# Kernel optimization log

Measured on AMD Instinct MI355X. Metric: run time of the kernel, lower is better.

The kernel has to match this reference:

```python
import jax, jax.numpy as jnp
import numpy as np
import math

THETA = 10000.0

def apply_rope(x):
    # x: [B, H, S, D] with D even; interleaved even/odd rotation
    B, H, S, D = x.shape
    dim_half = D // 2
    freq_idx = jnp.arange(dim_half, dtype=jnp.float32)
    inv_freq = jnp.exp(-math.log(THETA) * freq_idx * 2.0 / D)  # [D/2]
    pos = jnp.arange(S, dtype=jnp.float32)
    angles = pos[:, None] * inv_freq[None, :]      # [S, D/2]
    cos = jnp.cos(angles)[None, None]              # [1,1,S,D/2]
    sin = jnp.sin(angles)[None, None]
    x_even = x[..., ::2]
    x_odd = x[..., 1::2]
    r_even = x_even * cos - x_odd * sin
    r_odd = x_odd * cos + x_even * sin
    return jnp.stack([r_even, r_odd], axis=-1).reshape(B, H, S, D)

def setup_inputs() -> dict:
    key = jax.random.key(0)
    ks = jax.random.split(key, 5)
    B, S, E = 2, 2048, 1024
    std = 0.02
    inp = {
        "hidden_states": jax.random.normal(ks[0], (B, S, E), dtype=jnp.float32),
        "Wq": jax.random.normal(ks[1], (E, E), dtype=jnp.float32) * std,
        "bq": jnp.zeros((E,), dtype=jnp.float32),
        "Wk": jax.random.normal(ks[2], (E, E), dtype=jnp.float32) * std,
        "bk": jnp.zeros((E,), dtype=jnp.float32),
        "Wv": jax.random.normal(ks[3], (E, E), dtype=jnp.float32) * std,
        "bv": jnp.zeros((E,), dtype=jnp.float32),
        "Wo": jax.random.normal(ks[4], (E, E), dtype=jnp.float32) * std,
        "bo": jnp.zeros((E,), dtype=jnp.float32),
    }
    return inp

def reference(hidden_states, Wq, bq, Wk, bk, Wv, bv, Wo, bo):
    NUM_HEADS = 16
    B, S, E = hidden_states.shape
    D = E // NUM_HEADS
    scale = 1.0 / math.sqrt(D)

    def proj(W, b):
        # torch Linear: x @ W.T + b; then [B,S,H,D] -> [B,H,S,D]
        y = hidden_states @ W.T + b
        return y.reshape(B, S, NUM_HEADS, D).transpose(0, 2, 1, 3)

    q = apply_rope(proj(Wq, bq))
    k = apply_rope(proj(Wk, bk))
    v = proj(Wv, bv)

    scores = jnp.einsum("bhqd,bhkd->bhqk", q, k) * scale
    attn = jax.nn.softmax(scores, axis=-1)
    out = jnp.einsum("bhqk,bhkd->bhqd", attn, v)  # [B,H,S,D]
    out = out.transpose(0, 2, 1, 3).reshape(B, S, E)
    return out @ Wo.T + bo  # dropout: eval mode (identity)
```

## Files before the change

kernel.cpp:

```cpp
#include <hip/hip_runtime.h>
#include <hip/hip_bf16.h>
#include <math.h>

#define B_ 2
#define S_ 2048
#define E_ 1024
#define H_ 16
#define D_ 64
#define M_ (B_*S_)
#define PT 32

typedef short bf16x8 __attribute__((ext_vector_type(8)));
typedef float f32x4 __attribute__((ext_vector_type(4)));
typedef unsigned short u16x4 __attribute__((ext_vector_type(4)));

#define SCLQ 0.18033688011112042f

__device__ __forceinline__ unsigned short f2bf(float f) {
    unsigned int u = __builtin_bit_cast(unsigned int, f);
    u += 0x7FFFu + ((u >> 16) & 1u);
    return (unsigned short)(u >> 16);
}
__device__ __forceinline__ unsigned int pk2bf(float a, float b) {
    __hip_bfloat162 h = __float22bfloat162_rn(make_float2(a, b));
    unsigned int u;
    __builtin_memcpy(&u, &h, 4);
    return u;
}
__device__ __forceinline__ f32x4 mfma16(bf16x8 a, bf16x8 b, f32x4 c) {
    return __builtin_amdgcn_mfma_f32_16x16x32_bf16(a, b, c, 0, 0, 0);
}
__device__ __forceinline__ bf16x8 cvt8(const float* p) {
    f32x4 lo = *(const f32x4*)p;
    f32x4 hi = *(const f32x4*)(p + 4);
    unsigned int pk[4];
    pk[0] = pk2bf(lo[0], lo[1]);
    pk[1] = pk2bf(lo[2], lo[3]);
    pk[2] = pk2bf(hi[0], hi[1]);
    pk[3] = pk2bf(hi[2], hi[3]);
    bf16x8 r;
    __builtin_memcpy(&r, pk, 16);
    return r;
}
__device__ __forceinline__ void g2l16(const unsigned short* g, unsigned short* l) {
    __builtin_amdgcn_global_load_lds(
        (const __attribute__((address_space(1))) unsigned int*)(const void*)g,
        (__attribute__((address_space(3))) unsigned int*)(void*)l,
        16, 0, 0);
}

__global__ __launch_bounds__(256) void cvt_kernel(
    const float* __restrict__ X,  const float* __restrict__ Wq,
    const float* __restrict__ Wk, const float* __restrict__ Wv,
    const float* __restrict__ Wo,
    unsigned short* __restrict__ Xb, unsigned short* __restrict__ Wb,
    float* __restrict__ tab)
{
    const int y = blockIdx.y;
    if (y == 5) {
        unsigned int i = blockIdx.x * 256 + threadIdx.x;
        if (i < 32 * 2048) {
            int f = i >> 11, s = i & 2047;
            const float C = -0.41524101186091903f;
            const float INV2PI = 0.15915494309189535f;
            float inv_rev = exp2f(C * (float)f) * INV2PI;
            float rev = (float)s * inv_rev;
            float fr = rev - rintf(rev);
            tab[i]           = __builtin_amdgcn_cosf(fr);
            tab[65536 + i]   = __builtin_amdgcn_sinf(fr);
        }
        return;
    }
    const float* src = (y == 0) ? X : (y == 1) ? Wq : (y == 2) ? Wk : (y == 3) ? Wv : Wo;
    unsigned short* dst = (y == 0) ? Xb : Wb + (size_t)(y - 1) * (E_ * E_);
    const size_t n = (y == 0) ? (size_t)M_ * E_ : (size_t)E_ * E_;
    size_t i = ((size_t)blockIdx.x * 256 + threadIdx.x) * 8;
    if (i < n) *(bf16x8*)(dst + i) = cvt8(src + i);
}

__global__ __launch_bounds__(256, 4) void qkv_rope_bf(
    const unsigned short* __restrict__ Xb, const unsigned short* __restrict__ Wb,
    const float* __restrict__ bq, const float* __restrict__ bk,
    const float* __restrict__ bv, const float* __restrict__ tab,
    unsigned short* __restrict__ Qo, unsigned short* __restrict__ Ko,
    unsigned short* __restrict__ Vo)
{
    __shared__ __align__(16) unsigned char lds_raw[128 * 132 * 2];
    unsigned short* As = (unsigned short*)lds_raw;
    unsigned short* Bs = (unsigned short*)(lds_raw + 16384);
    unsigned short* Cs = (unsigned short*)lds_raw;

    const int t = threadIdx.x;
    const int w = t >> 6, lane = t & 63, quad = lane >> 4, l16 = lane & 15;
    const int wr = (w >> 1) * 64, wc = (w & 1) * 64;

    const int wgid = blockIdx.x + ((blockIdx.y + (blockIdx.z << 5)) << 3);
    const int sw = (wgid & 7) * 96 + (wgid >> 3);
    const int n0 = (sw & 7) * 128;
    const int rem = sw >> 3;
    const int m0 = (rem & 31) * 128;
    const int z = rem >> 5;

    const unsigned short* W = Wb + (size_t)z * (E_ * E_);
    const float* bias = (z == 0) ? bq : (z == 1) ? bk : bv;

    const int r8 = t >> 3;
    const int scol = ((t & 7) ^ ((t >> 3) & 7)) * 8;
    const unsigned short* Ag = Xb + (size_t)(m0 + r8) * E_ + scol;
    const unsigned short* Bg = W  + (size_t)(n0 + r8) * E_ + scol;

    const int sw0 = ((quad)     ^ (l16 & 7)) * 8;
    const int sw1 = ((4 + quad) ^ (l16 & 7)) * 8;

    f32x4 zero = {0.f, 0.f, 0.f, 0.f};
    f32x4 acc[4][4];
#pragma unroll
    for (int i = 0; i < 4; i++)
#pragma unroll
        for (int j = 0; j < 4; j++) acc[i][j] = zero;

    for (int kt = 0; kt < E_; kt += 64) {
        __syncthreads();
#pragma unroll
        for (int c = 0; c < 4; c++) {
            g2l16(Ag + kt + (size_t)(c * 32) * E_, &As[t * 8 + c * 2048]);
            g2l16(Bg + kt + (size_t)(c * 32) * E_, &Bs[t * 8 + c * 2048]);
        }
        __syncthreads();
#pragma unroll
        for (int ks = 0; ks < 2; ks++) {
            const int so = ks ? sw1 : sw0;
            bf16x8 af[4], bfr[4];
#pragma unroll
            for (int i = 0; i < 4; i++)
                af[i] = *(const bf16x8*)&As[(wr + i * 16 + l16) * 64 + so];
#pragma unroll
            for (int j = 0; j < 4; j++)
                bfr[j] = *(const bf16x8*)&Bs[(wc + j * 16 + l16) * 64 + so];
#pragma unroll
            for (int i = 0; i < 4; i++)
#pragma unroll
                for (int j = 0; j < 4; j++)
                    acc[i][j] = mfma16(af[i], bfr[j], acc[i][j]);
        }
    }

    __syncthreads();
    const int seg = quad;
    if (z < 2) {
        const float qscale = (z == 0) ? SCLQ : 1.0f;
#pragma unroll
        for (int j = 0; j < 4; j++) {
            int n_local = wc + j * 16 + l16;
            int n = n0 + n_local;
            int d = n & 63, f = d >> 1;
            float bvv = bias[n];
            float sgn = (d & 1) ? 1.f : -1.f;
            const float* ct = tab + f * 2048;
            const float* st_ = tab + 65536 + f * 2048;
#pragma unroll
            for (int i = 0; i < 4; i++) {
                int mb = wr + i * 16 + quad * 4;
                int sb = (m0 + mb) & (S_ - 1);
                f32x4 cs4 = *(const f32x4*)&ct[sb];
                f32x4 sn4 = *(const f32x4*)&st_[sb];
#pragma unroll
                for (int r = 0; r < 4; r++) {
                    float val = acc[i][j][r] + bvv;
                    float oth = __shfl_xor(val, 1);
                    Cs[(mb + r) * 132 + n_local] =
                        f2bf((val * cs4[r] + sgn * oth * sn4[r]) * qscale);
                }
            }
        }
        __syncthreads();
        unsigned short* Out = (z == 0) ? Qo : Ko;
        const int btok = m0 >> 11;
        const int half = seg & 1;
#pragma unroll
        for (int it = 0; it < 16; it++) {
            int m_local = it * 8 + w * 2 + (seg >> 1);
            int s = (m0 + m_local) & (S_ - 1);
            int h = (n0 + half * 64) >> 6;
            u16x4 v = *(const u16x4*)&Cs[m_local * 132 + half * 64 + l16 * 4];
            *(u16x4*)&Out[(((size_t)btok * H_ + h) * S_ + s) * D_ + l16 * 4] = v;
        }
    } else {
#pragma unroll
        for (int j = 0; j < 4; j++) {
            int n_local = wc + j * 16 + l16;
            float bvv = bias[n0 + n_local];
#pragma unroll
            for (int i = 0; i < 4; i++) {
                int mb = wr + i * 16 + quad * 4;
#pragma unroll
                for (int r = 0; r < 4; r++)
                    Cs[n_local * 132 + mb + r] = f2bf(acc[i][j][r] + bvv);
            }
        }
        __syncthreads();
        const int btok = m0 >> 11;
        const int s0 = m0 & (S_ - 1);
        const int half = seg & 1;
#pragma unroll
        for (int it = 0; it < 16; it++) {
            int n_local = it * 8 + w * 2 + (seg >> 1);
            int n = n0 + n_local;
            int h = n >> 6, d = n & 63;
            u16x4 v = *(const u16x4*)&Cs[n_local * 132 + half * 64 + l16 * 4];
            *(u16x4*)&Vo[(((size_t)btok * H_ + h) * D_ + d) * S_ + s0 + half * 64 + l16 * 4] = v;
        }
    }
}

__global__ __launch_bounds__(512, 2) void attn_direct(
    const unsigned short* __restrict__ Q, const unsigned short* __restrict__ K,
    const unsigned short* __restrict__ Vt, unsigned short* __restrict__ ctx)
{
    __shared__ unsigned short Ks[3][64 * 64];
    __shared__ unsigned short Vs[3][64 * 64];
    __shared__ unsigned short Ps[8][16 * 72];
    const int t = threadIdx.x;
    const int w = t >> 6, lane = t & 63, quad = lane >> 4, l16 = lane & 15;

    const int wgid = blockIdx.x + (blockIdx.y << 4);
    const int sw = (wgid & 7) * 64 + (wgid >> 3);
    const int bh = sw >> 4;
    const int q0 = (sw & 15) * 128 + w * 16;
    const int NT = S_ / 64;

    const unsigned short* Qg = Q + ((size_t)bh * S_ + q0) * D_;
    bf16x8 qf[2];
#pragma unroll
    for (int ks = 0; ks < 2; ks++)
        qf[ks] = *(const bf16x8*)(Qg + (size_t)l16 * 64 + ks * 32 + quad * 8);

    bf16x8 ones;
#pragma unroll
    for (int e = 0; e < 8; e++) ones[e] = (short)0x3F80;

    f32x4 zero = {0.f, 0.f, 0.f, 0.f};
    f32x4 acc_o[4];
    f32x4 acc_l = zero;
#pragma unroll
    for (int j = 0; j < 4; j++) acc_o[j] = zero;

    const int tt = t & 255, ksel = t >> 8;
    const int sr = tt >> 2;
    const int sc = ((tt & 3) ^ ((tt >> 3) & 3)) * 8;
    const unsigned short* KgL = K  + (size_t)bh * S_ * D_ + (size_t)sr * 64 + ksel * 32 + sc;
    const unsigned short* VgL = Vt + (size_t)bh * D_ * S_ + (size_t)sr * S_ + ksel * 32 + sc;

    const int sl = (quad ^ ((l16 >> 1) & 3)) * 8;

    g2l16(KgL, &Ks[0][t * 8]);
    g2l16(VgL, &Vs[0][t * 8]);
    __syncthreads();
    g2l16(KgL + 4096, &Ks[1][t * 8]);
    g2l16(VgL + 64,   &Vs[1][t * 8]);
    {
        f32x4 sc4[4];
#pragma unroll
        for (int j = 0; j < 4; j++) sc4[j] = zero;
#pragma unroll
        for (int ks = 0; ks < 2; ks++)
#pragma unroll
            for (int j = 0; j < 4; j++) {
                bf16x8 kf = *(const bf16x8*)&Ks[0][ks * 2048 + (j * 16 + l16) * 32 + sl];
                sc4[j] = mfma16(qf[ks], kf, sc4[j]);
            }
#pragma unroll
        for (int j = 0; j < 4; j++)
#pragma unroll
            for (int r = 0; r < 4; r += 2) {
                float pa = __builtin_amdgcn_exp2f(sc4[j][r]);
                float pb = __builtin_amdgcn_exp2f(sc4[j][r + 1]);
                unsigned int u = pk2bf(pa, pb);
                Ps[w][(quad * 4 + r)     * 72 + j * 16 + l16] = (unsigned short)u;
                Ps[w][(quad * 4 + r + 1) * 72 + j * 16 + l16] = (unsigned short)(u >> 16);
            }
    }

    int bc = 0, bn = 1, bx = 2;
    for (int i = 0; i < NT - 1; ++i) {
        __syncthreads();
        if (i + 2 < NT) {
            g2l16(KgL + (size_t)(i + 2) * 4096, &Ks[bx][t * 8]);
            g2l16(VgL + (i + 2) * 64,           &Vs[bx][t * 8]);
        }
        bf16x8 pf0 = *(const bf16x8*)&Ps[w][l16 * 72 + quad * 8];
        bf16x8 pf1 = *(const bf16x8*)&Ps[w][l16 * 72 + 32 + quad * 8];

        __builtin_amdgcn_s_setprio(1);
        f32x4 scn[4];
#pragma unroll
        for (int j = 0; j < 4; j++) scn[j] = zero;
#pragma unroll
        for (int ks = 0; ks < 2; ks++)
#pragma unroll
            for (int j = 0; j < 4; j++) {
                bf16x8 kf = *(const bf16x8*)&Ks[bn][ks * 2048 + (j * 16 + l16) * 32 + sl];
                scn[j] = mfma16(qf[ks], kf, scn[j]);
            }
#pragma unroll
        for (int jd = 0; jd < 4; jd++) {
            bf16x8 vf = *(const bf16x8*)&Vs[bc][(jd * 16 + l16) * 32 + sl];
            acc_o[jd] = mfma16(pf0, vf, acc_o[jd]);
        }
        acc_l = mfma16(pf0, ones, acc_l);
#pragma unroll
        for (int jd = 0; jd < 4; jd++) {
            bf16x8 vf = *(const bf16x8*)&Vs[bc][2048 + (jd * 16 + l16) * 32 + sl];
            acc_o[jd] = mfma16(pf1, vf, acc_o[jd]);
        }
        acc_l = mfma16(pf1, ones, acc_l);
        __builtin_amdgcn_s_setprio(0);

#pragma unroll
        for (int j = 0; j < 4; j++)
#pragma unroll
            for (int r = 0; r < 4; r += 2) {
                float pa = __builtin_amdgcn_exp2f(scn[j][r]);
                float pb = __builtin_amdgcn_exp2f(scn[j][r + 1]);
                unsigned int u = pk2bf(pa, pb);
                Ps[w][(quad * 4 + r)     * 72 + j * 16 + l16] = (unsigned short)u;
                Ps[w][(quad * 4 + r + 1) * 72 + j * 16 + l16] = (unsigned short)(u >> 16);
            }

        int tb = bc; bc = bn; bn = bx; bx = tb;
    }

    {
        bf16x8 pf0 = *(const bf16x8*)&Ps[w][l16 * 72 + quad * 8];
        bf16x8 pf1 = *(const bf16x8*)&Ps[w][l16 * 72 + 32 + quad * 8];
#pragma unroll
        for (int jd = 0; jd < 4; jd++) {
            bf16x8 vf = *(const bf16x8*)&Vs[bc][(jd * 16 + l16) * 32 + sl];
            acc_o[jd] = mfma16(pf0, vf, acc_o[jd]);
        }
        acc_l = mfma16(pf0, ones, acc_l);
#pragma unroll
        for (int jd = 0; jd < 4; jd++) {
            bf16x8 vf = *(const bf16x8*)&Vs[bc][2048 + (jd * 16 + l16) * 32 + sl];
            acc_o[jd] = mfma16(pf1, vf, acc_o[jd]);
        }
        acc_l = mfma16(pf1, ones, acc_l);
    }

    const int b = bh >> 4, h = bh & 15;
    f32x4 rl;
#pragma unroll
    for (int r = 0; r < 4; r++) rl[r] = 1.0f / acc_l[r];
#pragma unroll
    for (int jd = 0; jd < 4; jd++)
#pragma unroll
        for (int r = 0; r < 4; r++) {
            int qrow = q0 + quad * 4 + r;
            int col = h * 64 + jd * 16 + l16;
            ctx[((size_t)b * S_ + qrow) * E_ + col] = f2bf(acc_o[jd][r] * rl[r]);
        }
}

__global__ __launch_bounds__(256, 4) void out_bf(
    const unsigned short* __restrict__ Cx, const unsigned short* __restrict__ Wob,
    const float* __restrict__ bo, float* __restrict__ out)
{
    __shared__ unsigned short As[128 * 64];
    __shared__ unsigned short Bs[64 * 64];
    const int t = threadIdx.x;
    const int w = t >> 6, lane = t & 63, quad = lane >> 4, l16 = lane & 15;

    const int wgid = blockIdx.x + (blockIdx.y << 4);
    const int sw = (wgid & 7) * 64 + (wgid >> 3);
    const int n0 = (sw & 15) * 64;
    const int m0 = (sw >> 4) * 128;

    const int wr = w * 32;
    const int r8 = t >> 3;
    const int scol = ((t & 7) ^ ((t >> 3) & 7)) * 8;
    const unsigned short* Ag = Cx  + (size_t)(m0 + r8) * E_ + scol;
    const unsigned short* Bg = Wob + (size_t)(n0 + (r8 & 63)) * E_ + scol;

    const int sw0 = ((quad)     ^ (l16 & 7)) * 8;
    const int sw1 = ((4 + quad) ^ (l16 & 7)) * 8;

    f32x4 zero = {0.f, 0.f, 0.f, 0.f};
    f32x4 acc[2][4];
#pragma unroll
    for (int i = 0; i < 2; i++)
#pragma unroll
        for (int j = 0; j < 4; j++) acc[i][j] = zero;

    for (int kt = 0; kt < E_; kt += 64) {
        __syncthreads();
#pragma unroll
        for (int c = 0; c < 4; c++)
            g2l16(Ag + kt + (size_t)(c * 32) * E_, &As[t * 8 + c * 2048]);
#pragma unroll
        for (int c = 0; c < 2; c++)
            g2l16(Bg + kt + (size_t)(c * 32) * E_, &Bs[t * 8 + c * 2048]);
        __syncthreads();
#pragma unroll
        for (int ks = 0; ks < 2; ks++) {
            const int so = ks ? sw1 : sw0;
            bf16x8 af[2], bfr[4];
#pragma unroll
            for (int i = 0; i < 2; i++)
                af[i] = *(const bf16x8*)&As[(wr + i * 16 + l16) * 64 + so];
#pragma unroll
            for (int j = 0; j < 4; j++)
                bfr[j] = *(const bf16x8*)&Bs[(j * 16 + l16) * 64 + so];
#pragma unroll
            for (int i = 0; i < 2; i++)
#pragma unroll
                for (int j = 0; j < 4; j++)
                    acc[i][j] = mfma16(af[i], bfr[j], acc[i][j]);
        }
    }

#pragma unroll
    for (int j = 0; j < 4; j++) {
        int n = n0 + j * 16 + l16;
        float bvv = bo[n];
#pragma unroll
        for (int i = 0; i < 2; i++) {
            int mrow = m0 + wr + i * 16 + quad * 4;
#pragma unroll
            for (int r = 0; r < 4; r++)
                out[(size_t)(mrow + r) * E_ + n] = acc[i][j][r] + bvv;
        }
    }
}

__global__ __launch_bounds__(256, 3) void qkv_rope_f32(
    const float* __restrict__ X,
    const float* __restrict__ Wq, const float* __restrict__ Wk,
    const float* __restrict__ Wv,
    const float* __restrict__ bq, const float* __restrict__ bk,
    const float* __restrict__ bv,
    unsigned short* __restrict__ Qo, unsigned short* __restrict__ Ko,
    unsigned short* __restrict__ Vo)
{
    __shared__ __align__(16) unsigned char lds_raw[128 * 132 * 2];
    unsigned short* As = (unsigned short*)lds_raw;
    unsigned short* Bs = (unsigned short*)(lds_raw + 8192);
    unsigned short* Cs = (unsigned short*)lds_raw;

    const int t = threadIdx.x;
    const int w = t >> 6, lane = t & 63, quad = lane >> 4, l16 = lane & 15;
    const int wr = (w >> 1) * 64, wc = (w & 1) * 64;
    const int n0 = blockIdx.x * 128, m0 = blockIdx.y * 128;
    const int z = blockIdx.z;
    const float* W    = (z == 0) ? Wq : (z == 1) ? Wk : Wv;
    const float* bias = (z == 0) ? bq : (z == 1) ? bk : bv;

    const int r4 = t >> 2, c8 = (t & 3) * 8;
    const int st = r4 * PT + c8;
    const float* Ag = X + (size_t)(m0 + r4) * E_ + c8;
    const float* Bg = W + (size_t)(n0 + r4) * E_ + c8;

    f32x4 zero = {0.f, 0.f, 0.f, 0.f};
    f32x4 acc[4][4];
#pragma unroll
    for (int i = 0; i < 4; i++)
#pragma unroll
        for (int j = 0; j < 4; j++) acc[i][j] = zero;

    for (int kt = 0; kt < E_; kt += 32) {
        bf16x8 a0 = cvt8(Ag + kt);
        bf16x8 a1 = cvt8(Ag + 64 * E_ + kt);
        bf16x8 b0 = cvt8(Bg + kt);
        bf16x8 b1 = cvt8(Bg + 64 * E_ + kt);
        __syncthreads();
        *(bf16x8*)&As[st]           = a0;
        *(bf16x8*)&As[st + 64 * PT] = a1;
        *(bf16x8*)&Bs[st]           = b0;
        *(bf16x8*)&Bs[st + 64 * PT] = b1;
        __syncthreads();
        bf16x8 af[4], bfr[4];
#pragma unroll
        for (int i = 0; i < 4; i++)
            af[i] = *(const bf16x8*)&As[(wr + i * 16 + l16) * PT + quad * 8];
#pragma unroll
        for (int j = 0; j < 4; j++)
            bfr[j] = *(const bf16x8*)&Bs[(wc + j * 16 + l16) * PT + quad * 8];
#pragma unroll
        for (int i = 0; i < 4; i++)
#pragma unroll
            for (int j = 0; j < 4; j++)
                acc[i][j] = mfma16(af[i], bfr[j], acc[i][j]);
    }

    __syncthreads();
    const int seg = quad;
    if (z < 2) {
        const float C = -0.41524101186091903f;
        const float INV2PI = 0.15915494309189535f;
        const float qscale = (z == 0) ? SCLQ : 1.0f;
#pragma unroll
        for (int j = 0; j < 4; j++) {
            int n_local = wc + j * 16 + l16;
            int n = n0 + n_local;
            int d = n & 63, f = d >> 1;
            float inv_rev = exp2f(C * (float)f) * INV2PI;
            float bvv = bias[n];
            float sgn = (d & 1) ? 1.f : -1.f;
#pragma unroll
            for (int i = 0; i < 4; i++) {
                int mb = wr + i * 16 + quad * 4;
#pragma unroll
                for (int r = 0; r < 4; r++) {
                    int m = m0 + mb + r;
                    int s = m & (S_ - 1);
                    float val = acc[i][j][r] + bvv;
                    float oth = __shfl_xor(val, 1);
                    float rev = (float)s * inv_rev;
                    float fr = rev - rintf(rev);
                    float sn = __builtin_amdgcn_sinf(fr);
                    float cs = __builtin_amdgcn_cosf(fr);
                    Cs[(mb + r) * 132 + n_local] =
                        f2bf((val * cs + sgn * oth * sn) * qscale);
                }
            }
        }
        __syncthreads();
        unsigned short* Out = (z == 0) ? Qo : Ko;
        const int btok = m0 >> 11;
        const int half = seg & 1;
#pragma unroll
        for (int it = 0; it < 16; it++) {
            int m_local = it * 8 + w * 2 + (seg >> 1);
            int s = (m0 + m_local) & (S_ - 1);
            int h = (n0 + half * 64) >> 6;
            u16x4 v = *(const u16x4*)&Cs[m_local * 132 + half * 64 + l16 * 4];
            *(u16x4*)&Out[(((size_t)btok * H_ + h) * S_ + s) * D_ + l16 * 4] = v;
        }
    } else {
#pragma unroll
        for (int j = 0; j < 4; j++) {
            int n_local = wc + j * 16 + l16;
            float bvv = bias[n0 + n_local];
#pragma unroll
            for (int i = 0; i < 4; i++) {
                int mb = wr + i * 16 + quad * 4;
#pragma unroll
                for (int r = 0; r < 4; r++)
                    Cs[n_local * 132 + mb + r] = f2bf(acc[i][j][r] + bvv);
            }
        }
        __syncthreads();
        const int btok = m0 >> 11;
        const int s0 = m0 & (S_ - 1);
        const int half = seg & 1;
#pragma unroll
        for (int it = 0; it < 16; it++) {
            int n_local = it * 8 + w * 2 + (seg >> 1);
            int n = n0 + n_local;
            int h = n >> 6, d = n & 63;
            u16x4 v = *(const u16x4*)&Cs[n_local * 132 + half * 64 + l16 * 4];
            *(u16x4*)&Vo[(((size_t)btok * H_ + h) * D_ + d) * S_ + s0 + half * 64 + l16 * 4] = v;
        }
    }
}

__global__ __launch_bounds__(256, 2) void out_f32(
    const unsigned short* __restrict__ Cx, const float* __restrict__ Wo,
    const float* __restrict__ bo, float* __restrict__ out)
{
    __shared__ unsigned short As[128 * PT];
    __shared__ unsigned short Bs[64 * PT];
    const int t = threadIdx.x;
    const int w = t >> 6, lane = t & 63, quad = lane >> 4, l16 = lane & 15;
    const int m0 = blockIdx.y * 128, n0 = blockIdx.x * 64;
    const int wr = w * 32;
    const int r4 = t >> 2, c8 = (t & 3) * 8;
    const int st = r4 * PT + c8;
    const unsigned short* Ag = Cx + (size_t)(m0 + r4) * E_ + c8;
    const float*          Bg = Wo + (size_t)(n0 + (r4 & 63)) * E_ + c8;

    f32x4 zero = {0.f, 0.f, 0.f, 0.f};
    f32x4 acc[2][4];
#pragma unroll
    for (int i = 0; i < 2; i++)
#pragma unroll
        for (int j = 0; j < 4; j++) acc[i][j] = zero;

    for (int kt = 0; kt < E_; kt += 32) {
        bf16x8 a0 = *(const bf16x8*)(Ag + kt);
        bf16x8 a1 = *(const bf16x8*)(Ag + 64 * E_ + kt);
        bf16x8 b0 = cvt8(Bg + kt);
        __syncthreads();
        *(bf16x8*)&As[st]           = a0;
        *(bf16x8*)&As[st + 64 * PT] = a1;
        *(bf16x8*)&Bs[st]           = b0;
        __syncthreads();
        bf16x8 af[2], bfr[4];
#pragma unroll
        for (int i = 0; i < 2; i++)
            af[i] = *(const bf16x8*)&As[(wr + i * 16 + l16) * PT + quad * 8];
#pragma unroll
        for (int j = 0; j < 4; j++)
            bfr[j] = *(const bf16x8*)&Bs[(j * 16 + l16) * PT + quad * 8];
#pragma unroll
        for (int i = 0; i < 2; i++)
#pragma unroll
            for (int j = 0; j < 4; j++)
                acc[i][j] = mfma16(af[i], bfr[j], acc[i][j]);
    }

#pragma unroll
    for (int j = 0; j < 4; j++) {
        int n = n0 + j * 16 + l16;
        float bvv = bo[n];
#pragma unroll
        for (int i = 0; i < 2; i++) {
            int mrow = m0 + wr + i * 16 + quad * 4;
#pragma unroll
            for (int r = 0; r < 4; r++)
                out[(size_t)(mrow + r) * E_ + n] = acc[i][j][r] + bvv;
        }
    }
}

extern "C" void kernel_launch(void* const* d_in, const int* in_sizes, int n_in,
                              void* d_out, int out_size, void* d_ws, size_t ws_size,
                              hipStream_t stream) {
    const float* X  = (const float*)d_in[0];
    const float* Wq = (const float*)d_in[1];
    const float* bq = (const float*)d_in[2];
    const float* Wk = (const float*)d_in[3];
    const float* bk = (const float*)d_in[4];
    const float* Wv = (const float*)d_in[5];
    const float* bv = (const float*)d_in[6];
    const float* Wo = (const float*)d_in[7];
    const float* bo = (const float*)d_in[8];
    float* outp = (float*)d_out;

    const size_t TN = (size_t)B_ * H_ * S_ * D_;
    const size_t need_f32 = 4 * TN * sizeof(unsigned short);
    const size_t need_bf  = 5 * TN * sizeof(unsigned short) + 2 * 65536 * sizeof(float);
    if (ws_size < need_f32) return;

    unsigned short* Qb = (unsigned short*)d_ws;
    unsigned short* Kb = Qb + TN;
    unsigned short* Vb = Kb + TN;

    if (ws_size >= need_bf) {
        unsigned short* Xb = Vb + TN;
        unsigned short* Wb = Xb + TN;
        float* tab = (float*)(Wb + 4 * (size_t)(E_ * E_));
        unsigned short* Cx = Xb;

        cvt_kernel<<<dim3(2048, 6), 256, 0, stream>>>(X, Wq, Wk, Wv, Wo, Xb, Wb, tab);
        qkv_rope_bf<<<dim3(E_ / 128, M_ / 128, 3), 256, 0, stream>>>(
            Xb, Wb, bq, bk, bv, tab, Qb, Kb, Vb);
        attn_direct<<<dim3(S_ / 128, B_ * H_), 512, 0, stream>>>(Qb, Kb, Vb, Cx);
        out_bf<<<dim3(E_ / 64, M_ / 128), 256, 0, stream>>>(
            Cx, Wb + 3 * (size_t)(E_ * E_), bo, outp);
    } else {
        unsigned short* Cx = Vb + TN;
        qkv_rope_f32<<<dim3(E_ / 128, M_ / 128, 3), 256, 0, stream>>>(
            X, Wq, Wk, Wv, bq, bk, bv, Qb, Kb, Vb);
        attn_direct<<<dim3(S_ / 128, B_ * H_), 512, 0, stream>>>(Qb, Kb, Vb, Cx);
        out_f32<<<dim3(E_ / 64, M_ / 128), 256, 0, stream>>>(Cx, Wo, bo, outp);
    }
}
```

Before: 194.5 us.

## Keep softmax probabilities in registers via transposed QK^T MFMA layout

Computes the score tile transposed (K as the A operand) so each lane's MFMA output already matches the B-operand layout of a 16x16x16 bf16 MFMA. Exponentiated probabilities are packed straight into registers and fed to the PV product, removing the per-wave LDS staging buffer along with its store/load round trip. V fragments are read as 4-element chunks with new swizzled offsets, and the row-sum and output store are adapted to the transposed accumulator layout. The trade-off is twice as many, smaller MFMA instructions for the PV step and narrower LDS reads of V.

```diff
diff --git a/kernel.cpp b/kernel.cpp
--- a/kernel.cpp
+++ b/kernel.cpp
@@ -11,6 +11,7 @@
 #define PT 32
 
 typedef short bf16x8 __attribute__((ext_vector_type(8)));
+typedef short bf16x4 __attribute__((ext_vector_type(4)));
 typedef float f32x4 __attribute__((ext_vector_type(4)));
 typedef unsigned short u16x4 __attribute__((ext_vector_type(4)));
 
@@ -29,6 +30,17 @@
 }
 __device__ __forceinline__ f32x4 mfma16(bf16x8 a, bf16x8 b, f32x4 c) {
     return __builtin_amdgcn_mfma_f32_16x16x32_bf16(a, b, c, 0, 0, 0);
+}
+__device__ __forceinline__ f32x4 mfma16h(bf16x4 a, bf16x4 b, f32x4 c) {
+    return __builtin_amdgcn_mfma_f32_16x16x16bf16_1k(a, b, c, 0, 0, 0);
+}
+__device__ __forceinline__ bf16x4 pack4(float a, float b, float c, float d) {
+    unsigned int u[2];
+    u[0] = pk2bf(a, b);
+    u[1] = pk2bf(c, d);
+    bf16x4 r;
+    __builtin_memcpy(&r, u, 8);
+    return r;
 }
 __device__ __forceinline__ bf16x8 cvt8(const float* p) {
     f32x4 lo = *(const f32x4*)p;
@@ -219,14 +231,13 @@
 {
     __shared__ unsigned short Ks[3][64 * 64];
     __shared__ unsigned short Vs[3][64 * 64];
-    __shared__ unsigned short Ps[8][16 * 72];
     const int t = threadIdx.x;
     const int w = t >> 6, lane = t & 63, quad = lane >> 4, l16 = lane & 15;
 
     const int wgid = blockIdx.x + (blockIdx.y << 4);
-    const int sw = (wgid & 7) * 64 + (wgid >> 3);
-    const int bh = sw >> 4;
-    const int q0 = (sw & 15) * 128 + w * 16;
+    const int swz = (wgid & 7) * 64 + (wgid >> 3);
+    const int bh = swz >> 4;
+    const int q0 = (swz & 15) * 128 + w * 16;
     const int NT = S_ / 64;
 
     const unsigned short* Qg = Q + ((size_t)bh * S_ + q0) * D_;
@@ -235,9 +246,9 @@
     for (int ks = 0; ks < 2; ks++)
         qf[ks] = *(const bf16x8*)(Qg + (size_t)l16 * 64 + ks * 32 + quad * 8);
 
-    bf16x8 ones;
-#pragma unroll
-    for (int e = 0; e < 8; e++) ones[e] = (short)0x3F80;
+    bf16x4 ones4;
+#pragma unroll
+    for (int e = 0; e < 4; e++) ones4[e] = (short)0x3F80;
 
     f32x4 zero = {0.f, 0.f, 0.f, 0.f};
     f32x4 acc_o[4];
@@ -252,33 +263,37 @@
     const unsigned short* VgL = Vt + (size_t)bh * D_ * S_ + (size_t)sr * S_ + ksel * 32 + sc;
 
     const int sl = (quad ^ ((l16 >> 1) & 3)) * 8;
+    int vofs[4];
+#pragma unroll
+    for (int j = 0; j < 4; j++)
+        vofs[j] = (j >> 1) * 2048 +
+                  ((((j & 1) * 2 + (quad >> 1)) ^ ((l16 >> 1) & 3)) * 8) +
+                  (quad & 1) * 4;
 
     g2l16(KgL, &Ks[0][t * 8]);
     g2l16(VgL, &Vs[0][t * 8]);
     __syncthreads();
     g2l16(KgL + 4096, &Ks[1][t * 8]);
     g2l16(VgL + 64,   &Vs[1][t * 8]);
+
+    bf16x4 pfc[4];
     {
-        f32x4 sc4[4];
-#pragma unroll
-        for (int j = 0; j < 4; j++) sc4[j] = zero;
+        f32x4 st[4];
+#pragma unroll
+        for (int j = 0; j < 4; j++) st[j] = zero;
 #pragma unroll
         for (int ks = 0; ks < 2; ks++)
 #pragma unroll
             for (int j = 0; j < 4; j++) {
                 bf16x8 kf = *(const bf16x8*)&Ks[0][ks * 2048 + (j * 16 + l16) * 32 + sl];
-                sc4[j] = mfma16(qf[ks], kf, sc4[j]);
+                st[j] = mfma16(kf, qf[ks], st[j]);
             }
 #pragma unroll
         for (int j = 0; j < 4; j++)
-#pragma unroll
-            for (int r = 0; r < 4; r += 2) {
-                float pa = __builtin_amdgcn_exp2f(sc4[j][r]);
-                float pb = __builtin_amdgcn_exp2f(sc4[j][r + 1]);
-                unsigned int u = pk2bf(pa, pb);
-                Ps[w][(quad * 4 + r)     * 72 + j * 16 + l16] = (unsigned short)u;
-                Ps[w][(quad * 4 + r + 1) * 72 + j * 16 + l16] = (unsigned short)(u >> 16);
-            }
+            pfc[j] = pack4(__builtin_amdgcn_exp2f(st[j][0]),
+                           __builtin_amdgcn_exp2f(st[j][1]),
+                           __builtin_amdgcn_exp2f(st[j][2]),
+                           __builtin_amdgcn_exp2f(st[j][3]));
     }
 
     int bc = 0, bn = 1, bx = 2;
@@ -288,77 +303,57 @@
             g2l16(KgL + (size_t)(i + 2) * 4096, &Ks[bx][t * 8]);
             g2l16(VgL + (i + 2) * 64,           &Vs[bx][t * 8]);
         }
-        bf16x8 pf0 = *(const bf16x8*)&Ps[w][l16 * 72 + quad * 8];
-        bf16x8 pf1 = *(const bf16x8*)&Ps[w][l16 * 72 + 32 + quad * 8];
 
         __builtin_amdgcn_s_setprio(1);
-        f32x4 scn[4];
-#pragma unroll
-        for (int j = 0; j < 4; j++) scn[j] = zero;
+        f32x4 stn[4];
+#pragma unroll
+        for (int j = 0; j < 4; j++) stn[j] = zero;
 #pragma unroll
         for (int ks = 0; ks < 2; ks++)
 #pragma unroll
             for (int j = 0; j < 4; j++) {
                 bf16x8 kf = *(const bf16x8*)&Ks[bn][ks * 2048 + (j * 16 + l16) * 32 + sl];
-                scn[j] = mfma16(qf[ks], kf, scn[j]);
+                stn[j] = mfma16(kf, qf[ks], stn[j]);
             }
 #pragma unroll
+        for (int j = 0; j < 4; j++) {
+#pragma unroll
+            for (int jd = 0; jd < 4; jd++) {
+                bf16x4 vf = *(const bf16x4*)&Vs[bc][vofs[j] + (jd * 16 + l16) * 32];
+                acc_o[jd] = mfma16h(vf, pfc[j], acc_o[jd]);
+            }
+            acc_l = mfma16h(ones4, pfc[j], acc_l);
+        }
+        __builtin_amdgcn_s_setprio(0);
+
+#pragma unroll
+        for (int j = 0; j < 4; j++)
+            pfc[j] = pack4(__builtin_amdgcn_exp2f(stn[j][0]),
+                           __builtin_amdgcn_exp2f(stn[j][1]),
+                           __builtin_amdgcn_exp2f(stn[j][2]),
+                           __builtin_amdgcn_exp2f(stn[j][3]));
+
+        int tb = bc; bc = bn; bn = bx; bx = tb;
+    }
+
+#pragma unroll
+    for (int j = 0; j < 4; j++) {
+#pragma unroll
         for (int jd = 0; jd < 4; jd++) {
-            bf16x8 vf = *(const bf16x8*)&Vs[bc][(jd * 16 + l16) * 32 + sl];
-            acc_o[jd] = mfma16(pf0, vf, acc_o[jd]);
-        }
-        acc_l = mfma16(pf0, ones, acc_l);
-#pragma unroll
-        for (int jd = 0; jd < 4; jd++) {
-            bf16x8 vf = *(const bf16x8*)&Vs[bc][2048 + (jd * 16 + l16) * 32 + sl];
-            acc_o[jd] = mfma16(pf1, vf, acc_o[jd]);
-        }
-        acc_l = mfma16(pf1, ones, acc_l);
-        __builtin_amdgcn_s_setprio(0);
-
-#pragma unroll
-        for (int j = 0; j < 4; j++)
-#pragma unroll
-            for (int r = 0; r < 4; r += 2) {
-                float pa = __builtin_amdgcn_exp2f(scn[j][r]);
-                float pb = __builtin_amdgcn_exp2f(scn[j][r + 1]);
-                unsigned int u = pk2bf(pa, pb);
-                Ps[w][(quad * 4 + r)     * 72 + j * 16 + l16] = (unsigned short)u;
-                Ps[w][(quad * 4 + r + 1) * 72 + j * 16 + l16] = (unsigned short)(u >> 16);
-            }
-
-        int tb = bc; bc = bn; bn = bx; bx = tb;
-    }
-
-    {
-        bf16x8 pf0 = *(const bf16x8*)&Ps[w][l16 * 72 + quad * 8];
-        bf16x8 pf1 = *(const bf16x8*)&Ps[w][l16 * 72 + 32 + quad * 8];
-#pragma unroll
-        for (int jd = 0; jd < 4; jd++) {
-            bf16x8 vf = *(const bf16x8*)&Vs[bc][(jd * 16 + l16) * 32 + sl];
-            acc_o[jd] = mfma16(pf0, vf, acc_o[jd]);
-        }
-        acc_l = mfma16(pf0, ones, acc_l);
-#pragma unroll
-        for (int jd = 0; jd < 4; jd++) {
-            bf16x8 vf = *(const bf16x8*)&Vs[bc][2048 + (jd * 16 + l16) * 32 + sl];
-            acc_o[jd] = mfma16(pf1, vf, acc_o[jd]);
-        }
-        acc_l = mfma16(pf1, ones, acc_l);
+            bf16x4 vf = *(const bf16x4*)&Vs[bc][vofs[j] + (jd * 16 + l16) * 32];
+            acc_o[jd] = mfma16h(vf, pfc[j], acc_o[jd]);
+        }
+        acc_l = mfma16h(ones4, pfc[j], acc_l);
     }
 
     const int b = bh >> 4, h = bh & 15;
-    f32x4 rl;
-#pragma unroll
-    for (int r = 0; r < 4; r++) rl[r] = 1.0f / acc_l[r];
+    const float rl = 1.0f / acc_l[0];
+    const size_t rowbase = ((size_t)b * S_ + q0 + l16) * E_ + h * 64;
 #pragma unroll
     for (int jd = 0; jd < 4; jd++)
 #pragma unroll
-        for (int r = 0; r < 4; r++) {
-            int qrow = q0 + quad * 4 + r;
-            int col = h * 64 + jd * 16 + l16;
-            ctx[((size_t)b * S_ + qrow) * E_ + col] = f2bf(acc_o[jd][r] * rl[r]);
-        }
+        for (int r = 0; r < 4; r++)
+            ctx[rowbase + jd * 16 + quad * 4 + r] = f2bf(acc_o[jd][r] * rl);
 }
 
 __global__ __launch_bounds__(256, 4) void out_bf(
@@ -371,9 +366,9 @@
     const int w = t >> 6, lane = t & 63, quad = lane >> 4, l16 = lane & 15;
 
     const int wgid = blockIdx.x + (blockIdx.y << 4);
-    const int sw = (wgid & 7) * 64 + (wgid >> 3);
-    const int n0 = (sw & 15) * 64;
-    const int m0 = (sw >> 4) * 128;
+    const int swz = (wgid & 7) * 64 + (wgid >> 3);
+    const int n0 = (swz & 15) * 64;
+    const int m0 = (swz >> 4) * 128;
 
     const int wr = w * 32;
     const int r8 = t >> 3;
```

Measured after the change: 196.7 us. About the same (+1.1%).
